# Optimization experiments

Hardware: AMD Instinct MI355X
Metric: run time of the kernel (lower is better)

## Reference

```python
import jax, jax.numpy as jnp
import numpy as np

B = 524288

def setup_inputs() -> dict:
    key = jax.random.key(0)
    ks = jax.random.split(key, 9)
    return {
        "x":  jax.random.uniform(ks[0], (B, 1, 9, 9), dtype=jnp.float32),
        "Wc": jax.random.normal(ks[1], (81, 9), dtype=jnp.float32),
        "bc": jax.random.normal(ks[2], (81,), dtype=jnp.float32),
        "Wh": jax.random.normal(ks[3], (27, 9), dtype=jnp.float32),
        "bh": jax.random.normal(ks[4], (27,), dtype=jnp.float32),
        "Wm": jax.random.normal(ks[5], (12, 9), dtype=jnp.float32),
        "bm": jax.random.normal(ks[6], (12,), dtype=jnp.float32),
        "Wo": jax.random.normal(ks[7], (4, 4), dtype=jnp.float32),
        "bo": jax.random.normal(ks[8], (4,), dtype=jnp.float32),
    }

def _forward(x, Wc, bc, Wh, bh, Wm, bm, Wo, bo):
    b = x.shape[0]
    # 9 non-overlapping 3x3 patches (stride 3 over 9x9): (B, 9 patches, 9 pixels)
    p = x[:, 0].reshape(b, 3, 3, 3, 3).transpose(0, 1, 3, 2, 4).reshape(b, 9, 9)
    # conv layer: 9 logic kernels per patch -> (B, 9, 9) -> (B, 81)
    feat = jax.nn.sigmoid(
        jnp.einsum('bgp,gkp->bgk', p, Wc.reshape(9, 9, 9)) + bc.reshape(9, 9)
    ).reshape(b, 81)
    # hidden layer: 9 groups x 3 neurons, each over 9 inputs -> (B, 27)
    h = jax.nn.sigmoid(
        jnp.einsum('bgp,gnp->bgn', feat.reshape(b, 9, 9), Wh.reshape(9, 3, 9))
        + bh.reshape(9, 3)
    ).reshape(b, 27)
    # middle layer: 3 groups x 4 neurons, each over 9 inputs -> (B, 12)
    m = jax.nn.sigmoid(
        jnp.einsum('bgp,gnp->bgn', h.reshape(b, 3, 9), Wm.reshape(3, 4, 9))
        + bm.reshape(3, 4)
    ).reshape(b, 12)
    # output layer: class c reads middle group c % 3 (4 values each)
    num_classes = Wo.shape[0]
    grp = jnp.arange(num_classes) % 3                   # (C,)
    mg = m.reshape(b, 3, 4)[:, grp]                     # (B, C, 4)
    output_logits = jnp.einsum('bcp,cp->bc', mg, Wo) + bo
    return output_logits

def reference(x, Wc, bc, Wh, bh, Wm, bm, Wo, bo):
    return _forward(x, Wc, bc, Wh, bh, Wm, bm, Wo, bo)
```

## Files before the change

### kernel.cpp

```cpp
#include <hip/hip_runtime.h>

#define THREADS 256

__device__ __forceinline__ float fast_sigmoid(float v) {
    float e = __expf(-v);
    return __builtin_amdgcn_rcpf(1.0f + e);
}

__global__ __launch_bounds__(THREADS, 4) void olcnn_kernel(
    const float* __restrict__ x,
    const float* __restrict__ Wc, const float* __restrict__ bc,
    const float* __restrict__ Wh, const float* __restrict__ bh,
    const float* __restrict__ Wm, const float* __restrict__ bm,
    const float* __restrict__ Wo, const float* __restrict__ bo,
    float* __restrict__ out)
{
    const int s = blockIdx.x * THREADS + threadIdx.x;
    const float* xs = x + s * 81;

    float pix[81];
    #pragma unroll
    for (int i = 0; i < 81; ++i) pix[i] = xs[i];

    float res[4];

    #pragma unroll
    for (int G = 0; G < 3; ++G) {
        float hbuf[9];
        #pragma unroll
        for (int j = 0; j < 3; ++j) {
            const int g = G * 3 + j;
            float feat[9];
            #pragma unroll
            for (int k = 0; k < 9; ++k) {
                float acc = bc[g * 9 + k];
                #pragma unroll
                for (int pr = 0; pr < 3; ++pr)
                    #pragma unroll
                    for (int pc = 0; pc < 3; ++pc)
                        acc = fmaf(pix[G * 27 + pr * 9 + j * 3 + pc],
                                   Wc[(g * 9 + k) * 9 + pr * 3 + pc], acc);
                feat[k] = fast_sigmoid(acc);
            }
            #pragma unroll
            for (int n = 0; n < 3; ++n) {
                float acc = bh[g * 3 + n];
                #pragma unroll
                for (int p = 0; p < 9; ++p)
                    acc = fmaf(feat[p], Wh[(g * 3 + n) * 9 + p], acc);
                hbuf[j * 3 + n] = fast_sigmoid(acc);
            }
        }

        float m[4];
        #pragma unroll
        for (int n = 0; n < 4; ++n) {
            float acc = bm[G * 4 + n];
            #pragma unroll
            for (int p = 0; p < 9; ++p)
                acc = fmaf(hbuf[p], Wm[(G * 4 + n) * 9 + p], acc);
            m[n] = fast_sigmoid(acc);
        }

        {
            float acc = bo[G];
            #pragma unroll
            for (int p = 0; p < 4; ++p)
                acc = fmaf(m[p], Wo[G * 4 + p], acc);
            res[G] = acc;
        }
        if (G == 0) {
            float acc = bo[3];
            #pragma unroll
            for (int p = 0; p < 4; ++p)
                acc = fmaf(m[p], Wo[3 * 4 + p], acc);
            res[3] = acc;
        }
    }

    float4 o;
    o.x = res[0]; o.y = res[1]; o.z = res[2]; o.w = res[3];
    ((float4*)out)[s] = o;
}

extern "C" void kernel_launch(void* const* d_in, const int* in_sizes, int n_in,
                              void* d_out, int out_size, void* d_ws, size_t ws_size,
                              hipStream_t stream) {
    const float* x  = (const float*)d_in[0];
    const float* Wc = (const float*)d_in[1];
    const float* bc = (const float*)d_in[2];
    const float* Wh = (const float*)d_in[3];
    const float* bh = (const float*)d_in[4];
    const float* Wm = (const float*)d_in[5];
    const float* bm = (const float*)d_in[6];
    const float* Wo = (const float*)d_in[7];
    const float* bo = (const float*)d_in[8];
    float* out = (float*)d_out;

    const int B = in_sizes[0] / 81;
    const int blocks = B / THREADS;
    olcnn_kernel<<<blocks, THREADS, 0, stream>>>(x, Wc, bc, Wh, bh, Wm, bm,
                                                 Wo, bo, out);
}
```

Before: 271.3 us.

## Process two samples per thread with rotating register buffers to overlap loads and compute

Each thread now handles two samples and splits each sample's 81 pixels into three 27-float row groups. Three rotating register buffers are filled with loads that are pinned ahead of the compute for the previous group using sched_barrier and asm fences, so memory latency is hidden by math on the other sample. Grid size is halved and launch bounds drop from 4 to 3 blocks per CU to leave room for the extra live registers. The risks are lower occupancy and compiler scheduling limits that could offset the overlap.

```diff
diff --git a/kernel.cpp b/kernel.cpp
--- a/kernel.cpp
+++ b/kernel.cpp
@@ -7,7 +7,64 @@
     return __builtin_amdgcn_rcpf(1.0f + e);
 }
 
-__global__ __launch_bounds__(THREADS, 4) void olcnn_kernel(
+template<int G>
+__device__ __forceinline__ void compute_group(
+    const float* __restrict__ p,
+    const float* __restrict__ Wc, const float* __restrict__ bc,
+    const float* __restrict__ Wh, const float* __restrict__ bh,
+    const float* __restrict__ Wm, const float* __restrict__ bm,
+    const float* __restrict__ Wo, const float* __restrict__ bo,
+    float& outA, float& outB)
+{
+    float hb[9];
+    #pragma unroll
+    for (int j = 0; j < 3; ++j) {
+        const int g = G * 3 + j;
+        float feat[9];
+        #pragma unroll
+        for (int k = 0; k < 9; ++k) {
+            float acc = bc[g * 9 + k];
+            #pragma unroll
+            for (int pr = 0; pr < 3; ++pr)
+                #pragma unroll
+                for (int pc = 0; pc < 3; ++pc)
+                    acc = fmaf(p[pr * 9 + j * 3 + pc],
+                               Wc[(g * 9 + k) * 9 + pr * 3 + pc], acc);
+            feat[k] = fast_sigmoid(acc);
+        }
+        #pragma unroll
+        for (int n = 0; n < 3; ++n) {
+            float acc = bh[g * 3 + n];
+            #pragma unroll
+            for (int pi = 0; pi < 9; ++pi)
+                acc = fmaf(feat[pi], Wh[(g * 3 + n) * 9 + pi], acc);
+            hb[j * 3 + n] = fast_sigmoid(acc);
+        }
+    }
+    float m[4];
+    #pragma unroll
+    for (int n = 0; n < 4; ++n) {
+        float acc = bm[G * 4 + n];
+        #pragma unroll
+        for (int pi = 0; pi < 9; ++pi)
+            acc = fmaf(hb[pi], Wm[(G * 4 + n) * 9 + pi], acc);
+        m[n] = fast_sigmoid(acc);
+    }
+    float acc = bo[G];
+    #pragma unroll
+    for (int pi = 0; pi < 4; ++pi)
+        acc = fmaf(m[pi], Wo[G * 4 + pi], acc);
+    outA = acc;
+    if (G == 0) {
+        float acc2 = bo[3];
+        #pragma unroll
+        for (int pi = 0; pi < 4; ++pi)
+            acc2 = fmaf(m[pi], Wo[12 + pi], acc2);
+        outB = acc2;
+    }
+}
+
+__global__ __launch_bounds__(THREADS, 3) void olcnn_kernel(
     const float* __restrict__ x,
     const float* __restrict__ Wc, const float* __restrict__ bc,
     const float* __restrict__ Wh, const float* __restrict__ bh,
@@ -15,72 +72,48 @@
     const float* __restrict__ Wo, const float* __restrict__ bo,
     float* __restrict__ out)
 {
-    const int s = blockIdx.x * THREADS + threadIdx.x;
-    const float* xs = x + s * 81;
+    const int tid = threadIdx.x;
+    const int s0  = blockIdx.x * (THREADS * 2) + tid;
+    const int s1  = s0 + THREADS;
+    const float* xa = x + s0 * 81;
+    const float* xb = x + s1 * 81;
 
-    float pix[81];
-    #pragma unroll
-    for (int i = 0; i < 81; ++i) pix[i] = xs[i];
+    float q0[27], q1[27], q2[27];
 
-    float res[4];
+#define LOADQ(Q, SRC, G) do { _Pragma("unroll")                        \
+    for (int i_ = 0; i_ < 27; ++i_) Q[i_] = (SRC)[(G) * 27 + i_]; } while (0)
+#define FENCE(Q) do { _Pragma("unroll")                                \
+    for (int i_ = 0; i_ < 27; ++i_) asm volatile("" : "+v"(Q[i_])); } while (0)
+#define SB() __builtin_amdgcn_sched_barrier(0)
 
-    #pragma unroll
-    for (int G = 0; G < 3; ++G) {
-        float hbuf[9];
-        #pragma unroll
-        for (int j = 0; j < 3; ++j) {
-            const int g = G * 3 + j;
-            float feat[9];
-            #pragma unroll
-            for (int k = 0; k < 9; ++k) {
-                float acc = bc[g * 9 + k];
-                #pragma unroll
-                for (int pr = 0; pr < 3; ++pr)
-                    #pragma unroll
-                    for (int pc = 0; pc < 3; ++pc)
-                        acc = fmaf(pix[G * 27 + pr * 9 + j * 3 + pc],
-                                   Wc[(g * 9 + k) * 9 + pr * 3 + pc], acc);
-                feat[k] = fast_sigmoid(acc);
-            }
-            #pragma unroll
-            for (int n = 0; n < 3; ++n) {
-                float acc = bh[g * 3 + n];
-                #pragma unroll
-                for (int p = 0; p < 9; ++p)
-                    acc = fmaf(feat[p], Wh[(g * 3 + n) * 9 + p], acc);
-                hbuf[j * 3 + n] = fast_sigmoid(acc);
-            }
-        }
+    float r0, r1, r2, r3, r4, r5, r6, r7;
 
-        float m[4];
-        #pragma unroll
-        for (int n = 0; n < 4; ++n) {
-            float acc = bm[G * 4 + n];
-            #pragma unroll
-            for (int p = 0; p < 9; ++p)
-                acc = fmaf(hbuf[p], Wm[(G * 4 + n) * 9 + p], acc);
-            m[n] = fast_sigmoid(acc);
-        }
+    LOADQ(q0, xa, 0); LOADQ(q1, xb, 0); SB();
 
-        {
-            float acc = bo[G];
-            #pragma unroll
-            for (int p = 0; p < 4; ++p)
-                acc = fmaf(m[p], Wo[G * 4 + p], acc);
-            res[G] = acc;
-        }
-        if (G == 0) {
-            float acc = bo[3];
-            #pragma unroll
-            for (int p = 0; p < 4; ++p)
-                acc = fmaf(m[p], Wo[3 * 4 + p], acc);
-            res[3] = acc;
-        }
-    }
+    LOADQ(q2, xa, 1); SB();
+    FENCE(q0); compute_group<0>(q0, Wc, bc, Wh, bh, Wm, bm, Wo, bo, r0, r3);
 
-    float4 o;
-    o.x = res[0]; o.y = res[1]; o.z = res[2]; o.w = res[3];
-    ((float4*)out)[s] = o;
+    LOADQ(q0, xb, 1); SB();
+    FENCE(q1); compute_group<0>(q1, Wc, bc, Wh, bh, Wm, bm, Wo, bo, r4, r7);
+
+    LOADQ(q1, xa, 2); SB();
+    FENCE(q2); compute_group<1>(q2, Wc, bc, Wh, bh, Wm, bm, Wo, bo, r1, r1);
+
+    LOADQ(q2, xb, 2); SB();
+    FENCE(q0); compute_group<1>(q0, Wc, bc, Wh, bh, Wm, bm, Wo, bo, r5, r5);
+
+    SB();
+    FENCE(q1); compute_group<2>(q1, Wc, bc, Wh, bh, Wm, bm, Wo, bo, r2, r2);
+    FENCE(q2); compute_group<2>(q2, Wc, bc, Wh, bh, Wm, bm, Wo, bo, r6, r6);
+
+#undef LOADQ
+#undef FENCE
+#undef SB
+
+    float4 oA; oA.x = r0; oA.y = r1; oA.z = r2; oA.w = r3;
+    float4 oB; oB.x = r4; oB.y = r5; oB.z = r6; oB.w = r7;
+    ((float4*)out)[s0] = oA;
+    ((float4*)out)[s1] = oB;
 }
 
 extern "C" void kernel_launch(void* const* d_in, const int* in_sizes, int n_in,
@@ -98,7 +131,7 @@
     float* out = (float*)d_out;
 
     const int B = in_sizes[0] / 81;
-    const int blocks = B / THREADS;
+    const int blocks = B / (THREADS * 2);
     olcnn_kernel<<<blocks, THREADS, 0, stream>>>(x, Wc, bc, Wh, bh, Wm, bm,
                                                  Wo, bo, out);
 }
```

Measured after the change: 297.1 us. 9.5% more time.
